# Kernel tuning notes

Measured on AMD Instinct MI355X. Metric: run time of the kernel, lower is better.

The kernel has to match this reference:

```python
import jax, jax.numpy as jnp
import numpy as np

N = 100000
K = 20
SCALES = (5, 10, 20)
D = 256  # dimoffeat


def _leaky(x):
    return jax.nn.leaky_relu(x, negative_slope=0.2)


def setup_inputs() -> dict:
    key = jax.random.key(0)
    ks = jax.random.split(key, 20)
    S = len(SCALES)
    inp = {
        "points": jax.random.normal(ks[0], (N, 3), dtype=jnp.float32),
        "neighbor_indices": jax.random.randint(ks[1], (N, K), 0, N, dtype=jnp.int64),
        # per-scale patch PointNet weights, stacked over the 3 scales
        "pw1": jax.random.normal(ks[2], (S, D // 4, 3), dtype=jnp.float32) * 0.05,
        "pb1": jax.random.normal(ks[3], (S, D // 4), dtype=jnp.float32) * 0.05,
        "pw2": jax.random.normal(ks[4], (S, D // 2, D // 4), dtype=jnp.float32) * 0.05,
        "pb2": jax.random.normal(ks[5], (S, D // 2), dtype=jnp.float32) * 0.05,
        "pw3": jax.random.normal(ks[6], (S, D, D // 2), dtype=jnp.float32) * 0.05,
        "pb3": jax.random.normal(ks[7], (S, D), dtype=jnp.float32) * 0.05,
        # shared MLP (all 1x1 convs == linears)
        "sw1": jax.random.normal(ks[8], (D, S * D), dtype=jnp.float32) * 0.05,
        "sb1": jax.random.normal(ks[9], (D,), dtype=jnp.float32) * 0.05,
        "sw2": jax.random.normal(ks[10], (D // 2, D), dtype=jnp.float32) * 0.05,
        "sb2": jax.random.normal(ks[11], (D // 2,), dtype=jnp.float32) * 0.05,
        "sw3": jax.random.normal(ks[12], (D // 4, D // 2), dtype=jnp.float32) * 0.05,
        "sb3": jax.random.normal(ks[13], (D // 4,), dtype=jnp.float32) * 0.05,
        "sw4": jax.random.normal(ks[14], (D // 8, D // 4), dtype=jnp.float32) * 0.05,
        "sb4": jax.random.normal(ks[15], (D // 8,), dtype=jnp.float32) * 0.05,
        "sw5": jax.random.normal(ks[16], (1, D // 8), dtype=jnp.float32) * 0.05,
        "sb5": jax.random.normal(ks[17], (1,), dtype=jnp.float32) * 0.05,
    }
    return inp


def reference(points, pw1, pb1, pw2, pb2, pw3, pb3,
              sw1, sb1, sw2, sb2, sw3, sb3, sw4, sb4, sw5, sb5,
              neighbor_indices):
    feats_list = []
    for i, s in enumerate(SCALES):
        # gather neighbors and center: [N, s, 3]
        nb = points[neighbor_indices[:, :s]] - points[:, None, :]
        # 1x1-conv MLP == per-point linear layers
        h = _leaky(jnp.einsum('nsc,dc->nsd', nb, pw1[i]) + pb1[i])
        h = _leaky(jnp.einsum('nsc,dc->nsd', h, pw2[i]) + pb2[i])
        h = jnp.einsum('nsc,dc->nsd', h, pw3[i]) + pb3[i]
        feats_list.append(jnp.max(h, axis=1))  # max-pool over neighbors -> [N, D]
    x = jnp.concatenate(feats_list, axis=1)  # [N, 3*D]
    h = _leaky(x @ sw1.T + sb1)
    h = _leaky(h @ sw2.T + sb2)
    h = _leaky(h @ sw3.T + sb3)
    h = _leaky(h @ sw4.T + sb4)
    out = h @ sw5.T + sb5  # [N, 1]
    return out[:, 0]
```

## Files before the change

kernel.cpp:

```cpp
#include <hip/hip_runtime.h>


typedef _Float16 f16x8 __attribute__((ext_vector_type(8)));
typedef _Float16 f16x4 __attribute__((ext_vector_type(4)));
typedef _Float16 f16x2 __attribute__((ext_vector_type(2)));
typedef __fp16   h16x2 __attribute__((ext_vector_type(2)));
typedef float    f32x4 __attribute__((ext_vector_type(4)));

#define PPB 32
#define KMAX 20

#define PW2OFF 0
#define PW3OFF 24576
#define SW1OFF 122880
#define SW2OFF 319488
#define SW3OFF 352256
#define SW4OFF 360448
#define PW1HOFF 362496
#define NFRAGS 708

#define NB_OFF 0
#define H1_OFF 10240
#define H2_OFF 33280
#define PW1H_OFF 76800
#define LDS_BYTES 77312
#define H1S 72
#define H2S 136
#define XIS 264
#define X2S 264
#define H3S 136
#define H4S 72
#define O4S 36

__device__ __forceinline__ float leakyf(float x) { return fmaxf(x, 0.2f * x); }

__device__ __forceinline__ f16x4 pkrtz4(f32x4 a) {
    h16x2 lo = __builtin_amdgcn_cvt_pkrtz(a[0], a[1]);
    h16x2 hi = __builtin_amdgcn_cvt_pkrtz(a[2], a[3]);
    f16x4 r;
    r[0] = (_Float16)lo[0]; r[1] = (_Float16)lo[1];
    r[2] = (_Float16)hi[0]; r[3] = (_Float16)hi[1];
    return r;
}
__device__ __forceinline__ f16x4 leaky4h(f16x4 h) {
    f16x4 s = h * (_Float16)0.2f;
    return __builtin_elementwise_max(h, s);
}
__device__ __forceinline__ f16x4 rne4(f32x4 a) {
    f16x4 r; r[0] = (_Float16)a[0]; r[1] = (_Float16)a[1];
    r[2] = (_Float16)a[2]; r[3] = (_Float16)a[3];
    return r;
}
__device__ __forceinline__ f32x4 ldbias4(const float* b) {
    float4 t = *(const float4*)b;
    return (f32x4){t.x, t.y, t.z, t.w};
}

struct PrepRegion { const float* src; int inC; int Kk; int fEnd; int dstOff; };
struct PrepParams {
    PrepRegion r[10];
    const float* pw1; const float* pb1;
    _Float16* dst;
};

__global__ __launch_bounds__(256) void prep_kernel(PrepParams pp) {
    int gid = blockIdx.x * 256 + threadIdx.x;
    if (gid < NFRAGS * 64) {
        int f = gid >> 6, L = gid & 63;
        int ri = 0;
        while (f >= pp.r[ri].fEnd) ri++;
        int f0 = (ri == 0) ? 0 : pp.r[ri - 1].fEnd;
        const PrepRegion R = pp.r[ri];
        int fl = f - f0;
        int nt = fl / R.Kk, kk = fl - nt * R.Kk;
        int row = nt * 16 + (L & 15);
        int col = kk * 32 + (L >> 4) * 8;
        const float* s = R.src + row * R.inC + col;
        f16x8 v;
#pragma unroll
        for (int j = 0; j < 8; ++j) v[j] = (_Float16)s[j];
        *(f16x8*)(pp.dst + R.dstOff + fl * 512 + L * 8) = v;
    } else if (gid < NFRAGS * 64 + 96) {
        int t = gid - NFRAGS * 64;
        int i = t >> 5, pr = t & 31;
        int c0 = pr * 2, c1 = pr * 2 + 1;
        f16x8 v;
        v[0] = (_Float16)pp.pw1[i * 192 + c0 * 3 + 0];
        v[1] = (_Float16)pp.pw1[i * 192 + c1 * 3 + 0];
        v[2] = (_Float16)pp.pw1[i * 192 + c0 * 3 + 1];
        v[3] = (_Float16)pp.pw1[i * 192 + c1 * 3 + 1];
        v[4] = (_Float16)pp.pw1[i * 192 + c0 * 3 + 2];
        v[5] = (_Float16)pp.pw1[i * 192 + c1 * 3 + 2];
        v[6] = (_Float16)pp.pb1[i * 64 + c0];
        v[7] = (_Float16)pp.pb1[i * 64 + c1];
        *(f16x8*)(pp.dst + PW1HOFF + (i * 32 + pr) * 8) = v;
    }
}

struct MainParams {
    const float* points; const int* nidx;
    const float* pb2; const float* pb3;
    const float* sb1; const float* sb2; const float* sb3; const float* sb4;
    const float* sw5; const float* sb5;
    const _Float16* wsH;
    float* out;
    int n;
};

__global__ __launch_bounds__(256, 2) void msp_mfma(MainParams p) {
    __shared__ __align__(16) unsigned char pool[LDS_BYTES];
    float*    nbf = (float*)(pool + NB_OFF);
    _Float16* h1  = (_Float16*)(pool + H1_OFF);
    _Float16* h2  = (_Float16*)(pool + H2_OFF);
    _Float16* xi  = (_Float16*)(pool + H2_OFF);
    _Float16* x2  = (_Float16*)(pool + H1_OFF);
    _Float16* h3  = (_Float16*)(pool + NB_OFF);
    _Float16* h4  = (_Float16*)(pool + H2_OFF);
    float*    out4= (float*)(pool + H2_OFF + 8192);
    _Float16* pw1h= (_Float16*)(pool + PW1H_OFF);

    const int tid  = threadIdx.x;
    const int wave = tid >> 6, lane = tid & 63;
    const int q = lane >> 4, m16 = lane & 15;
    const int n0 = blockIdx.x * PPB;

    for (int r = tid; r < PPB * KMAX; r += 256) {
        int pp_ = r & 31, k = r >> 5;
        int idx = p.nidx[(n0 + pp_) * KMAX + k];
        const float* npt = p.points + idx * 3;
        const float* cpt = p.points + (n0 + pp_) * 3;
        float4 v;
        v.x = npt[0] - cpt[0];
        v.y = npt[1] - cpt[1];
        v.z = npt[2] - cpt[2];
        v.w = 1.0f;
        ((float4*)nbf)[r] = v;
    }

    f32x4 accC[2][4];
#pragma unroll
    for (int mt = 0; mt < 4; ++mt) {
        f32x4 b = ldbias4(p.sb1 + (wave * 4 + mt) * 16 + q * 4);
        accC[0][mt] = b; accC[1][mt] = b;
    }
    __syncthreads();

    const int NC[3] = {1, 2, 4};
    for (int i = 0; i < 3; ++i) {
        if (tid < 32)
            ((f16x8*)pw1h)[tid] = ((const f16x8*)(p.wsH + PW1HOFF))[i * 32 + tid];

        f16x8 W2f[2][2], W3f[4][4];
#pragma unroll
        for (int mt = 0; mt < 2; ++mt)
#pragma unroll
            for (int kk = 0; kk < 2; ++kk)
                W2f[mt][kk] = *(const f16x8*)(p.wsH + PW2OFF +
                    (i * 16 + (wave * 2 + mt) * 2 + kk) * 512 + lane * 8);
#pragma unroll
        for (int mt = 0; mt < 4; ++mt)
#pragma unroll
            for (int kk = 0; kk < 4; ++kk)
                W3f[mt][kk] = *(const f16x8*)(p.wsH + PW3OFF +
                    (i * 64 + (wave * 4 + mt) * 4 + kk) * 512 + lane * 8);

        f32x4 b2v[2];
#pragma unroll
        for (int mt = 0; mt < 2; ++mt)
            b2v[mt] = ldbias4(p.pb2 + i * 128 + (wave * 2 + mt) * 16 + q * 4);

        f32x4 maxC[2][4];
#pragma unroll
        for (int pt = 0; pt < 2; ++pt)
#pragma unroll
            for (int mt = 0; mt < 4; ++mt)
                maxC[pt][mt] = (f32x4){-3.0e38f, -3.0e38f, -3.0e38f, -3.0e38f};

        __syncthreads();

        for (int c = 0; c < NC[i]; ++c) {
            const int k0 = c * 5;
            {
                int p_ = tid & 31, g = tid >> 5;
#pragma unroll
                for (int kc = 0; kc < 5; ++kc) {
                    float4 nv = ((const float4*)nbf)[(k0 + kc) * 32 + p_];
                    f16x2 X; X[0] = X[1] = (_Float16)nv.x;
                    f16x2 Y; Y[0] = Y[1] = (_Float16)nv.y;
                    f16x2 Z; Z[0] = Z[1] = (_Float16)nv.z;
                    f16x8 hv;
#pragma unroll
                    for (int j = 0; j < 4; ++j) {
                        f16x8 w8 = ((const f16x8*)pw1h)[g * 4 + j];
                        f16x2 wx = {w8[0], w8[1]}, wy = {w8[2], w8[3]};
                        f16x2 wz = {w8[4], w8[5]}, wb = {w8[6], w8[7]};
                        f16x2 v = wx * X + wy * Y + wz * Z + wb;
                        f16x2 s = v * (_Float16)0.2f;
                        v = __builtin_elementwise_max(v, s);
                        hv[2 * j] = v[0]; hv[2 * j + 1] = v[1];
                    }
                    *(f16x8*)(h1 + (kc * 32 + p_) * H1S + g * 8) = hv;
                }
            }
            __syncthreads();

            for (int nt = 0; nt < 10; ++nt) {
                const _Float16* br = h1 + (nt * 16 + m16) * H1S + q * 8;
                f16x8 b0 = *(const f16x8*)br;
                f16x8 b1 = *(const f16x8*)(br + 32);
                f32x4 acc0 = __builtin_amdgcn_mfma_f32_16x16x32_f16(W2f[0][0], b0, b2v[0], 0, 0, 0);
                f32x4 acc1 = __builtin_amdgcn_mfma_f32_16x16x32_f16(W2f[1][0], b0, b2v[1], 0, 0, 0);
                acc0 = __builtin_amdgcn_mfma_f32_16x16x32_f16(W2f[0][1], b1, acc0, 0, 0, 0);
                acc1 = __builtin_amdgcn_mfma_f32_16x16x32_f16(W2f[1][1], b1, acc1, 0, 0, 0);
                _Float16* wr = h2 + (nt * 16 + m16) * H2S + q * 4;
                *(f16x4*)(wr + (wave * 2 + 0) * 16) = leaky4h(pkrtz4(acc0));
                *(f16x4*)(wr + (wave * 2 + 1) * 16) = leaky4h(pkrtz4(acc1));
            }
            __syncthreads();

            for (int nt = 0; nt < 10; ++nt) {
                const _Float16* br = h2 + (nt * 16 + m16) * H2S + q * 8;
                f16x8 b[4];
#pragma unroll
                for (int kk = 0; kk < 4; ++kk) b[kk] = *(const f16x8*)(br + kk * 32);
                f32x4 acc[4];
#pragma unroll
                for (int mt = 0; mt < 4; ++mt)
                    acc[mt] = __builtin_amdgcn_mfma_f32_16x16x32_f16(W3f[mt][0], b[0],
                              (f32x4){0.f, 0.f, 0.f, 0.f}, 0, 0, 0);
#pragma unroll
                for (int kk = 1; kk < 4; ++kk)
#pragma unroll
                    for (int mt = 0; mt < 4; ++mt)
                        acc[mt] = __builtin_amdgcn_mfma_f32_16x16x32_f16(W3f[mt][kk], b[kk], acc[mt], 0, 0, 0);
                int pt = nt & 1;
#pragma unroll
                for (int mt = 0; mt < 4; ++mt)
                    maxC[pt][mt] = __builtin_elementwise_max(maxC[pt][mt], acc[mt]);
            }
            __syncthreads();
        }

#pragma unroll
        for (int pt = 0; pt < 2; ++pt)
#pragma unroll
            for (int mt = 0; mt < 4; ++mt) {
                f32x4 b3 = ldbias4(p.pb3 + i * 256 + (wave * 4 + mt) * 16 + q * 4);
                *(f16x4*)(xi + (pt * 16 + m16) * XIS + (wave * 4 + mt) * 16 + q * 4)
                    = rne4(maxC[pt][mt] + b3);
            }
        __syncthreads();

        for (int nt = 0; nt < 2; ++nt) {
            const _Float16* br = xi + (nt * 16 + m16) * XIS + q * 8;
            f16x8 bf[8];
#pragma unroll
            for (int kk = 0; kk < 8; ++kk) bf[kk] = *(const f16x8*)(br + kk * 32);
#pragma unroll
            for (int kk = 0; kk < 8; ++kk)
#pragma unroll
                for (int mt = 0; mt < 4; ++mt) {
                    f16x8 a = *(const f16x8*)(p.wsH + SW1OFF +
                        ((wave * 4 + mt) * 24 + i * 8 + kk) * 512 + lane * 8);
                    accC[nt][mt] = __builtin_amdgcn_mfma_f32_16x16x32_f16(a, bf[kk], accC[nt][mt], 0, 0, 0);
                }
        }
        __syncthreads();
    }

#pragma unroll
    for (int nt = 0; nt < 2; ++nt)
#pragma unroll
        for (int mt = 0; mt < 4; ++mt) {
            f32x4 v = accC[nt][mt];
#pragma unroll
            for (int r = 0; r < 4; ++r) v[r] = leakyf(v[r]);
            *(f16x4*)(x2 + (nt * 16 + m16) * X2S + (wave * 4 + mt) * 16 + q * 4) = rne4(v);
        }
    __syncthreads();

    for (int nt = 0; nt < 2; ++nt) {
        const _Float16* br = x2 + (nt * 16 + m16) * X2S + q * 8;
        f16x8 bf[8];
#pragma unroll
        for (int kk = 0; kk < 8; ++kk) bf[kk] = *(const f16x8*)(br + kk * 32);
        f32x4 acc[2];
#pragma unroll
        for (int mt = 0; mt < 2; ++mt)
            acc[mt] = ldbias4(p.sb2 + (wave * 2 + mt) * 16 + q * 4);
#pragma unroll
        for (int kk = 0; kk < 8; ++kk)
#pragma unroll
            for (int mt = 0; mt < 2; ++mt) {
                f16x8 a = *(const f16x8*)(p.wsH + SW2OFF +
                    ((wave * 2 + mt) * 8 + kk) * 512 + lane * 8);
                acc[mt] = __builtin_amdgcn_mfma_f32_16x16x32_f16(a, bf[kk], acc[mt], 0, 0, 0);
            }
#pragma unroll
        for (int mt = 0; mt < 2; ++mt) {
            f32x4 v = acc[mt];
#pragma unroll
            for (int r = 0; r < 4; ++r) v[r] = leakyf(v[r]);
            *(f16x4*)(h3 + (nt * 16 + m16) * H3S + (wave * 2 + mt) * 16 + q * 4) = rne4(v);
        }
    }
    __syncthreads();

    for (int nt = 0; nt < 2; ++nt) {
        const _Float16* br = h3 + (nt * 16 + m16) * H3S + q * 8;
        f32x4 acc = ldbias4(p.sb3 + wave * 16 + q * 4);
#pragma unroll
        for (int kk = 0; kk < 4; ++kk) {
            f16x8 bf = *(const f16x8*)(br + kk * 32);
            f16x8 a = *(const f16x8*)(p.wsH + SW3OFF + (wave * 4 + kk) * 512 + lane * 8);
            acc = __builtin_amdgcn_mfma_f32_16x16x32_f16(a, bf, acc, 0, 0, 0);
        }
#pragma unroll
        for (int r = 0; r < 4; ++r) acc[r] = leakyf(acc[r]);
        *(f16x4*)(h4 + (nt * 16 + m16) * H4S + wave * 16 + q * 4) = rne4(acc);
    }
    __syncthreads();

    if (wave < 2) {
        for (int nt = 0; nt < 2; ++nt) {
            const _Float16* br = h4 + (nt * 16 + m16) * H4S + q * 8;
            f32x4 acc = ldbias4(p.sb4 + wave * 16 + q * 4);
#pragma unroll
            for (int kk = 0; kk < 2; ++kk) {
                f16x8 bf = *(const f16x8*)(br + kk * 32);
                f16x8 a = *(const f16x8*)(p.wsH + SW4OFF + (wave * 2 + kk) * 512 + lane * 8);
                acc = __builtin_amdgcn_mfma_f32_16x16x32_f16(a, bf, acc, 0, 0, 0);
            }
#pragma unroll
            for (int r = 0; r < 4; ++r) acc[r] = leakyf(acc[r]);
            *(f32x4*)(out4 + (nt * 16 + m16) * O4S + wave * 16 + q * 4) = acc;
        }
    }
    __syncthreads();

    if (tid < PPB) {
        float acc = p.sb5[0];
#pragma unroll
        for (int c = 0; c < 32; ++c)
            acc = fmaf(out4[tid * O4S + c], p.sw5[c], acc);
        p.out[n0 + tid] = acc;
    }
}

extern "C" void kernel_launch(void* const* d_in, const int* in_sizes, int n_in,
                              void* d_out, int out_size, void* d_ws, size_t ws_size,
                              hipStream_t stream) {
    const float* points = (const float*)d_in[0];
    const int*   nidx   = (const int*)d_in[1];
    const float* pw1 = (const float*)d_in[2];  const float* pb1 = (const float*)d_in[3];
    const float* pw2 = (const float*)d_in[4];  const float* pb2 = (const float*)d_in[5];
    const float* pw3 = (const float*)d_in[6];  const float* pb3 = (const float*)d_in[7];
    const float* sw1 = (const float*)d_in[8];  const float* sb1 = (const float*)d_in[9];
    const float* sw2 = (const float*)d_in[10]; const float* sb2 = (const float*)d_in[11];
    const float* sw3 = (const float*)d_in[12]; const float* sb3 = (const float*)d_in[13];
    const float* sw4 = (const float*)d_in[14]; const float* sb4 = (const float*)d_in[15];
    const float* sw5 = (const float*)d_in[16]; const float* sb5 = (const float*)d_in[17];

    _Float16* wsH = (_Float16*)d_ws;

    PrepParams pp;
    for (int i = 0; i < 3; ++i)
        pp.r[i] = { pw2 + i * 8192, 64, 2, 16 * (i + 1), PW2OFF + i * 8192 };
    for (int i = 0; i < 3; ++i)
        pp.r[3 + i] = { pw3 + i * 32768, 128, 4, 48 + 64 * (i + 1), PW3OFF + i * 32768 };
    pp.r[6] = { sw1, 768, 24, 624, SW1OFF };
    pp.r[7] = { sw2, 256, 8, 688, SW2OFF };
    pp.r[8] = { sw3, 128, 4, 704, SW3OFF };
    pp.r[9] = { sw4, 64, 2, 708, SW4OFF };
    pp.pw1 = pw1; pp.pb1 = pb1;
    pp.dst = wsH;

    int prep_threads = NFRAGS * 64 + 96;
    hipLaunchKernelGGL(prep_kernel, dim3((prep_threads + 255) / 256), dim3(256), 0, stream, pp);

    MainParams mp;
    mp.points = points; mp.nidx = nidx;
    mp.pb2 = pb2; mp.pb3 = pb3;
    mp.sb1 = sb1; mp.sb2 = sb2; mp.sb3 = sb3; mp.sb4 = sb4;
    mp.sw5 = sw5; mp.sb5 = sb5;
    mp.wsH = wsH;
    mp.out = (float*)d_out;
    mp.n = in_sizes[0] / 3;

    int blocks = mp.n / PPB;
    hipLaunchKernelGGL(msp_mfma, dim3(blocks), dim3(256), 0, stream, mp);
}
```

Baseline: 421.5 us.

## Switch layer-3 and shared-MLP first layer to 32x32x16 MFMA tiles

Replaces the 16x16x32 MFMA tiling for the per-scale pw3 layer and the sw1 layer with 32x32x16 MFMA, which changes the weight fragment layout in the prep kernel, the LDS read pattern and the accumulator and max-pool register layout. The larger tile raises arithmetic per LDS fragment load and reduces the number of MFMA instructions issued. In exchange, each wave holds 16-wide accumulators, which raises register pressure and could hurt occupancy under launch_bounds(256,2).

Result: slower. 463.2 us (+9.9%).

```diff
diff --git a/kernel.cpp b/kernel.cpp
--- a/kernel.cpp
+++ b/kernel.cpp
@@ -6,6 +6,7 @@
 typedef _Float16 f16x2 __attribute__((ext_vector_type(2)));
 typedef __fp16   h16x2 __attribute__((ext_vector_type(2)));
 typedef float    f32x4 __attribute__((ext_vector_type(4)));
+typedef float    f32x16 __attribute__((ext_vector_type(16)));
 
 #define PPB 32
 #define KMAX 20
@@ -56,7 +57,7 @@
     return (f32x4){t.x, t.y, t.z, t.w};
 }
 
-struct PrepRegion { const float* src; int inC; int Kk; int fEnd; int dstOff; };
+struct PrepRegion { const float* src; int inC; int Kk; int fEnd; int dstOff; int wide; };
 struct PrepParams {
     PrepRegion r[10];
     const float* pw1; const float* pb1;
@@ -73,8 +74,14 @@
         const PrepRegion R = pp.r[ri];
         int fl = f - f0;
         int nt = fl / R.Kk, kk = fl - nt * R.Kk;
-        int row = nt * 16 + (L & 15);
-        int col = kk * 32 + (L >> 4) * 8;
+        int row, col;
+        if (R.wide) {
+            row = nt * 32 + (L & 31);
+            col = kk * 16 + (L >> 5) * 8;
+        } else {
+            row = nt * 16 + (L & 15);
+            col = kk * 32 + (L >> 4) * 8;
+        }
         const float* s = R.src + row * R.inC + col;
         f16x8 v;
 #pragma unroll
@@ -122,6 +129,8 @@
     const int tid  = threadIdx.x;
     const int wave = tid >> 6, lane = tid & 63;
     const int q = lane >> 4, m16 = lane & 15;
+    const int l31 = lane & 31, hi = lane >> 5;
+    const int h8 = hi * 8, hi4 = hi * 4;
     const int n0 = blockIdx.x * PPB;
 
     for (int r = tid; r < PPB * KMAX; r += 256) {
@@ -137,12 +146,15 @@
         ((float4*)nbf)[r] = v;
     }
 
-    f32x4 accC[2][4];
-#pragma unroll
-    for (int mt = 0; mt < 4; ++mt) {
-        f32x4 b = ldbias4(p.sb1 + (wave * 4 + mt) * 16 + q * 4);
-        accC[0][mt] = b; accC[1][mt] = b;
-    }
+    f32x16 accC[2];
+#pragma unroll
+    for (int mt = 0; mt < 2; ++mt)
+#pragma unroll
+        for (int g = 0; g < 4; ++g) {
+            f32x4 b = ldbias4(p.sb1 + (wave * 2 + mt) * 32 + g * 8 + hi4);
+#pragma unroll
+            for (int j = 0; j < 4; ++j) accC[mt][g * 4 + j] = b[j];
+        }
     __syncthreads();
 
     const int NC[3] = {1, 2, 4};
@@ -150,7 +162,7 @@
         if (tid < 32)
             ((f16x8*)pw1h)[tid] = ((const f16x8*)(p.wsH + PW1HOFF))[i * 32 + tid];
 
-        f16x8 W2f[2][2], W3f[4][4];
+        f16x8 W2f[2][2], W3f[2][8];
 #pragma unroll
         for (int mt = 0; mt < 2; ++mt)
 #pragma unroll
@@ -158,23 +170,22 @@
                 W2f[mt][kk] = *(const f16x8*)(p.wsH + PW2OFF +
                     (i * 16 + (wave * 2 + mt) * 2 + kk) * 512 + lane * 8);
 #pragma unroll
-        for (int mt = 0; mt < 4; ++mt)
-#pragma unroll
-            for (int kk = 0; kk < 4; ++kk)
+        for (int mt = 0; mt < 2; ++mt)
+#pragma unroll
+            for (int kk = 0; kk < 8; ++kk)
                 W3f[mt][kk] = *(const f16x8*)(p.wsH + PW3OFF +
-                    (i * 64 + (wave * 4 + mt) * 4 + kk) * 512 + lane * 8);
+                    (i * 64 + (wave * 2 + mt) * 8 + kk) * 512 + lane * 8);
 
         f32x4 b2v[2];
 #pragma unroll
         for (int mt = 0; mt < 2; ++mt)
             b2v[mt] = ldbias4(p.pb2 + i * 128 + (wave * 2 + mt) * 16 + q * 4);
 
-        f32x4 maxC[2][4];
-#pragma unroll
-        for (int pt = 0; pt < 2; ++pt)
-#pragma unroll
-            for (int mt = 0; mt < 4; ++mt)
-                maxC[pt][mt] = (f32x4){-3.0e38f, -3.0e38f, -3.0e38f, -3.0e38f};
+        f32x16 maxC[2];
+#pragma unroll
+        for (int mt = 0; mt < 2; ++mt)
+#pragma unroll
+            for (int j = 0; j < 16; ++j) maxC[mt][j] = -3.0e38f;
 
         __syncthreads();
 
@@ -218,64 +229,62 @@
             }
             __syncthreads();
 
-            for (int nt = 0; nt < 10; ++nt) {
-                const _Float16* br = h2 + (nt * 16 + m16) * H2S + q * 8;
-                f16x8 b[4];
-#pragma unroll
-                for (int kk = 0; kk < 4; ++kk) b[kk] = *(const f16x8*)(br + kk * 32);
-                f32x4 acc[4];
-#pragma unroll
-                for (int mt = 0; mt < 4; ++mt)
-                    acc[mt] = __builtin_amdgcn_mfma_f32_16x16x32_f16(W3f[mt][0], b[0],
-                              (f32x4){0.f, 0.f, 0.f, 0.f}, 0, 0, 0);
-#pragma unroll
-                for (int kk = 1; kk < 4; ++kk)
-#pragma unroll
-                    for (int mt = 0; mt < 4; ++mt)
-                        acc[mt] = __builtin_amdgcn_mfma_f32_16x16x32_f16(W3f[mt][kk], b[kk], acc[mt], 0, 0, 0);
-                int pt = nt & 1;
-#pragma unroll
-                for (int mt = 0; mt < 4; ++mt)
-                    maxC[pt][mt] = __builtin_elementwise_max(maxC[pt][mt], acc[mt]);
+            for (int nt = 0; nt < 5; ++nt) {
+                const _Float16* br = h2 + (nt * 32 + l31) * H2S + h8;
+                f32x16 acc[2];
+                acc[0] = (f32x16){}; acc[1] = (f32x16){};
+#pragma unroll
+                for (int kk = 0; kk < 8; ++kk) {
+                    f16x8 bf = *(const f16x8*)(br + kk * 16);
+#pragma unroll
+                    for (int mt = 0; mt < 2; ++mt)
+                        acc[mt] = __builtin_amdgcn_mfma_f32_32x32x16_f16(W3f[mt][kk], bf, acc[mt], 0, 0, 0);
+                }
+#pragma unroll
+                for (int mt = 0; mt < 2; ++mt)
+                    maxC[mt] = __builtin_elementwise_max(maxC[mt], acc[mt]);
             }
             __syncthreads();
         }
 
 #pragma unroll
-        for (int pt = 0; pt < 2; ++pt)
-#pragma unroll
-            for (int mt = 0; mt < 4; ++mt) {
-                f32x4 b3 = ldbias4(p.pb3 + i * 256 + (wave * 4 + mt) * 16 + q * 4);
-                *(f16x4*)(xi + (pt * 16 + m16) * XIS + (wave * 4 + mt) * 16 + q * 4)
-                    = rne4(maxC[pt][mt] + b3);
+        for (int mt = 0; mt < 2; ++mt)
+#pragma unroll
+            for (int g = 0; g < 4; ++g) {
+                int ch = (wave * 2 + mt) * 32 + g * 8 + hi4;
+                f32x4 v;
+#pragma unroll
+                for (int j = 0; j < 4; ++j) v[j] = maxC[mt][g * 4 + j];
+                v = v + ldbias4(p.pb3 + i * 256 + ch);
+                *(f16x4*)(xi + l31 * XIS + ch) = rne4(v);
             }
         __syncthreads();
 
-        for (int nt = 0; nt < 2; ++nt) {
-            const _Float16* br = xi + (nt * 16 + m16) * XIS + q * 8;
-            f16x8 bf[8];
-#pragma unroll
-            for (int kk = 0; kk < 8; ++kk) bf[kk] = *(const f16x8*)(br + kk * 32);
-#pragma unroll
-            for (int kk = 0; kk < 8; ++kk)
-#pragma unroll
-                for (int mt = 0; mt < 4; ++mt) {
+        {
+            const _Float16* br = xi + l31 * XIS + h8;
+#pragma unroll
+            for (int kk = 0; kk < 16; ++kk) {
+                f16x8 bf = *(const f16x8*)(br + kk * 16);
+#pragma unroll
+                for (int mt = 0; mt < 2; ++mt) {
                     f16x8 a = *(const f16x8*)(p.wsH + SW1OFF +
-                        ((wave * 4 + mt) * 24 + i * 8 + kk) * 512 + lane * 8);
-                    accC[nt][mt] = __builtin_amdgcn_mfma_f32_16x16x32_f16(a, bf[kk], accC[nt][mt], 0, 0, 0);
+                        ((wave * 2 + mt) * 48 + i * 16 + kk) * 512 + lane * 8);
+                    accC[mt] = __builtin_amdgcn_mfma_f32_32x32x16_f16(a, bf, accC[mt], 0, 0, 0);
                 }
+            }
         }
         __syncthreads();
     }
 
 #pragma unroll
-    for (int nt = 0; nt < 2; ++nt)
-#pragma unroll
-        for (int mt = 0; mt < 4; ++mt) {
-            f32x4 v = accC[nt][mt];
-#pragma unroll
-            for (int r = 0; r < 4; ++r) v[r] = leakyf(v[r]);
-            *(f16x4*)(x2 + (nt * 16 + m16) * X2S + (wave * 4 + mt) * 16 + q * 4) = rne4(v);
+    for (int mt = 0; mt < 2; ++mt)
+#pragma unroll
+        for (int g = 0; g < 4; ++g) {
+            int ch = (wave * 2 + mt) * 32 + g * 8 + hi4;
+            f32x4 v;
+#pragma unroll
+            for (int j = 0; j < 4; ++j) v[j] = leakyf(accC[mt][g * 4 + j]);
+            *(f16x4*)(x2 + l31 * X2S + ch) = rne4(v);
         }
     __syncthreads();
 
@@ -365,13 +374,13 @@
 
     PrepParams pp;
     for (int i = 0; i < 3; ++i)
-        pp.r[i] = { pw2 + i * 8192, 64, 2, 16 * (i + 1), PW2OFF + i * 8192 };
+        pp.r[i] = { pw2 + i * 8192, 64, 2, 16 * (i + 1), PW2OFF + i * 8192, 0 };
     for (int i = 0; i < 3; ++i)
-        pp.r[3 + i] = { pw3 + i * 32768, 128, 4, 48 + 64 * (i + 1), PW3OFF + i * 32768 };
-    pp.r[6] = { sw1, 768, 24, 624, SW1OFF };
-    pp.r[7] = { sw2, 256, 8, 688, SW2OFF };
-    pp.r[8] = { sw3, 128, 4, 704, SW3OFF };
-    pp.r[9] = { sw4, 64, 2, 708, SW4OFF };
+        pp.r[3 + i] = { pw3 + i * 32768, 128, 8, 48 + 64 * (i + 1), PW3OFF + i * 32768, 1 };
+    pp.r[6] = { sw1, 768, 48, 624, SW1OFF, 1 };
+    pp.r[7] = { sw2, 256, 8, 688, SW2OFF, 0 };
+    pp.r[8] = { sw3, 128, 4, 704, SW3OFF, 0 };
+    pp.r[9] = { sw4, 64, 2, 708, SW4OFF, 0 };
     pp.pw1 = pw1; pp.pb1 = pb1;
     pp.dst = wsH;
 
```
